# Kernel optimization log

Hardware: AMD Instinct MI355X
Metric: run time of the kernel (lower is better)

## Reference

```python
import jax, jax.numpy as jnp
import numpy as np

B, T, D, UNITS = 16, 4096, 1024, 1024


def setup_inputs() -> dict:
    key = jax.random.key(0)
    k1, k2 = jax.random.split(key)
    inputs = jax.random.normal(k1, (B, T, D), dtype=jnp.float32)
    att_keral = jax.random.normal(k2, (UNITS, D), dtype=jnp.float32) * 0.02
    return {"inputs": inputs, "att_keral": att_keral}


def reference(inputs, att_keral):
    # scores[b,t,u] = inputs[b,t,d] * att_keral[u,d] / sqrt(D)
    d = inputs.shape[-1]
    scale = 1.0 / jnp.sqrt(jnp.asarray(d, dtype=jnp.float32))
    scores = jnp.einsum('btd,ud->btu', inputs, att_keral) * scale
    # NOTE: the original computes alpha = softmax(scores) but (for isfinal=False)
    # multiplies the *scaled scores* (not alpha) back with att_keral. We reproduce
    # that exact math (alpha is dead code on this path).
    out = jnp.einsum('btu,ud->btd', scores, att_keral)
    return out
```

## Files before the change

### kernel.cpp

```cpp
#include <hip/hip_runtime.h>


typedef unsigned short u16;
typedef unsigned int u32;
typedef __bf16 bf16x8 __attribute__((ext_vector_type(8)));
typedef float f32x4 __attribute__((ext_vector_type(4)));

#define BAR() __builtin_amdgcn_s_barrier()
#define LGKM0() asm volatile("s_waitcnt lgkmcnt(0)" ::: "memory")
#define VMC(n) asm volatile("s_waitcnt vmcnt(" #n ")" ::: "memory")
#define SCHED0() __builtin_amdgcn_sched_barrier(0)

__device__ __forceinline__ u16 f2bf(float f) {
  u32 u = __float_as_uint(f);
  u += 0x7fffu + ((u >> 16) & 1u);
  return (u16)(u >> 16);
}

__device__ __forceinline__ void gload_lds16(const void* g, void* l) {
  __builtin_amdgcn_global_load_lds((const __attribute__((address_space(1))) u32*)g,
                                   (__attribute__((address_space(3))) u32*)l,
                                   16, 0, 0);
}

__device__ __forceinline__ void load2x16(const float* p, f32x4& a, f32x4& b) {
  asm volatile("global_load_dwordx4 %0, %2, off\n\t"
               "global_load_dwordx4 %1, %2, off offset:16"
               : "=&v"(a), "=&v"(b)
               : "v"(p)
               : "memory");
}

__device__ __forceinline__ bf16x8 cvt8(f32x4 a, f32x4 b) {
  bf16x8 h;
  h[0] = (__bf16)a[0]; h[1] = (__bf16)a[1]; h[2] = (__bf16)a[2]; h[3] = (__bf16)a[3];
  h[4] = (__bf16)b[0]; h[5] = (__bf16)b[1]; h[6] = (__bf16)b[2]; h[7] = (__bf16)b[3];
  return h;
}

__global__ __launch_bounds__(256) void compute_M(const float* __restrict__ W,
                                                 u16* __restrict__ Mb) {
  __shared__ float w1[32][64];
  __shared__ float w2[32][64];
  const int t = threadIdx.x;
  const int i0 = blockIdx.y * 64;
  const int j0 = blockIdx.x * 64;
  const int tx = t & 15, ty = t >> 4;
  float acc[4][4] = {};
  for (int u0 = 0; u0 < 1024; u0 += 32) {
    __syncthreads();
#pragma unroll
    for (int p = 0; p < 2; ++p) {
      int idx = p * 256 + t;
      int lu = idx >> 4, lc = (idx & 15) * 4;
      *(float4*)&w1[lu][lc] = *(const float4*)(W + (size_t)(u0 + lu) * 1024 + i0 + lc);
      *(float4*)&w2[lu][lc] = *(const float4*)(W + (size_t)(u0 + lu) * 1024 + j0 + lc);
    }
    __syncthreads();
#pragma unroll 8
    for (int u = 0; u < 32; ++u) {
      float4 a = *(const float4*)&w1[u][ty * 4];
      float4 b = *(const float4*)&w2[u][tx * 4];
      float av[4] = {a.x, a.y, a.z, a.w};
      float bv[4] = {b.x, b.y, b.z, b.w};
#pragma unroll
      for (int e = 0; e < 4; ++e)
#pragma unroll
        for (int f = 0; f < 4; ++f)
          acc[e][f] += av[e] * bv[f];
    }
  }
  const float s = 0.03125f;
#pragma unroll
  for (int e = 0; e < 4; ++e) {
    ushort4 v;
    v.x = f2bf(acc[e][0] * s);
    v.y = f2bf(acc[e][1] * s);
    v.z = f2bf(acc[e][2] * s);
    v.w = f2bf(acc[e][3] * s);
    *(ushort4*)(Mb + (size_t)(i0 + ty * 4 + e) * 1024 + j0 + tx * 4) = v;
  }
}

__global__ __launch_bounds__(512, 4) void gemm_xm(const float* __restrict__ X,
                                                  const u16* __restrict__ Mb,
                                                  float* __restrict__ out) {
  __shared__ u16 lA[2][8192];
  __shared__ u16 lB[3][4096];

  const int p = blockIdx.x;
  const int wg = (p & 7) * 256 + (p >> 3);
  const int bm = wg >> 3;
  const int bn = wg & 7;
  const size_t r0 = (size_t)bm * 256;
  const int c0 = bn * 128;

  const int t = threadIdx.x;
  const int lane = t & 63;
  const int w = t >> 6;
  const int wr = w >> 1, wc = w & 1;
  const int fr = lane & 15;
  const int kc = lane >> 4;

  const int srow = t >> 2;
  const int scl = t & 3;
  const int csw = scl ^ ((srow >> 1) & 3);
  const float* aLo = X + (r0 + srow) * 1024 + scl * 8;
  const float* aHi = X + (r0 + 128 + srow) * 1024 + scl * 8;
  u16* wLo = &lA[0][srow * 32 + csw * 8];
  u16* wHi = &lA[0][(srow + 128) * 32 + csw * 8];
  const u16* gB = Mb + (size_t)(c0 + srow) * 1024 + csw * 8;
  const int slB = w * 512;

  f32x4 acc[4][4] = {};
  f32x4 pfa, pfb, pfc, pfd;
  f32x4 q0a, q0b, q0c, q0d;

  load2x16(aLo, q0a, q0b);
  load2x16(aHi, q0c, q0d);
  load2x16(aLo + 32, pfa, pfb);
  load2x16(aHi + 32, pfc, pfd);
  gload_lds16(gB, (void*)&lB[0][slB]);
  gload_lds16(gB + 32, (void*)&lB[1][slB]);
  VMC(1);
  SCHED0();
  *(bf16x8*)(wLo) = cvt8(q0a, q0b);
  *(bf16x8*)(wHi) = cvt8(q0c, q0d);
  LGKM0();
  BAR();

  int rbB = 0, wbB = 2;
  for (int j = 0; j < 32; ++j) {
    const u16* bA = &lA[j & 1][0];
    const u16* bB = &lB[rbB][0];

    VMC(1);
    SCHED0();
    if (j <= 30) {
      const int ab = ((j + 1) & 1) * 8192;
      *(bf16x8*)(wLo + ab) = cvt8(pfa, pfb);
      *(bf16x8*)(wHi + ab) = cvt8(pfc, pfd);
    }
    bf16x8 af[4], bf[4];
#pragma unroll
    for (int m = 0; m < 4; ++m) {
      const int row = wr * 64 + m * 16 + fr;
      const int cs = kc ^ ((row >> 1) & 3);
      af[m] = *(const bf16x8*)&bA[row * 32 + cs * 8];
    }
#pragma unroll
    for (int n = 0; n < 4; ++n) {
      const int row = wc * 64 + n * 16 + fr;
      const int cs = kc ^ ((row >> 1) & 3);
      bf[n] = *(const bf16x8*)&bB[row * 32 + cs * 8];
    }
    if (j <= 29) {
      load2x16(aLo + (j + 2) * 32, pfa, pfb);
      load2x16(aHi + (j + 2) * 32, pfc, pfd);
      gload_lds16(gB + (j + 2) * 32, (void*)&lB[wbB][slB]);
    }
    BAR();
    LGKM0();
    SCHED0();
    __builtin_amdgcn_s_setprio(1);
#pragma unroll
    for (int m = 0; m < 4; ++m)
#pragma unroll
      for (int n = 0; n < 4; ++n)
        acc[m][n] = __builtin_amdgcn_mfma_f32_16x16x32_bf16(af[m], bf[n],
                                                            acc[m][n], 0, 0, 0);
    __builtin_amdgcn_s_setprio(0);
    if (j <= 29) {
      VMC(5);
    } else if (j == 30) {
      VMC(0);
    }
    SCHED0();
    BAR();
    rbB = (rbB == 2) ? 0 : rbB + 1;
    wbB = (wbB == 2) ? 0 : wbB + 1;
  }

  const int ocol = lane & 15;
  const int orow = (lane >> 4) * 4;
#pragma unroll
  for (int m = 0; m < 4; ++m) {
    const size_t rbase = (r0 + wr * 64 + m * 16 + orow) * 1024;
#pragma unroll
    for (int n = 0; n < 4; ++n) {
      float* o = out + rbase + (c0 + wc * 64 + n * 16 + ocol);
      o[0] = acc[m][n][0];
      o[1024] = acc[m][n][1];
      o[2048] = acc[m][n][2];
      o[3072] = acc[m][n][3];
    }
  }
}

extern "C" void kernel_launch(void* const* d_in, const int* in_sizes, int n_in,
                              void* d_out, int out_size, void* d_ws, size_t ws_size,
                              hipStream_t stream) {
  const float* X = (const float*)d_in[0];
  const float* W = (const float*)d_in[1];
  float* out = (float*)d_out;
  u16* Mb = (u16*)d_ws;

  compute_M<<<dim3(16, 16), 256, 0, stream>>>(W, Mb);
  gemm_xm<<<2048, 512, 0, stream>>>(X, Mb, out);
}
```

Before: 307.9 us.

## Enlarge GEMM tile to 256x256 with 8-slot LDS ping-pong pipeline

```diff
diff --git a/kernel.cpp b/kernel.cpp
--- a/kernel.cpp
+++ b/kernel.cpp
@@ -82,110 +82,132 @@
   }
 }
 
-__global__ __launch_bounds__(512, 4) void gemm_xm(const float* __restrict__ X,
-                                                  const u16* __restrict__ Mb,
-                                                  float* __restrict__ out) {
-  __shared__ u16 lA[2][8192];
-  __shared__ u16 lB[3][4096];
+__global__ __launch_bounds__(512, 2) void gemm8p(const float* __restrict__ X,
+                                                 const u16* __restrict__ Mb,
+                                                 float* __restrict__ out) {
+  __shared__ u16 lds[8 * 8192];
 
   const int p = blockIdx.x;
-  const int wg = (p & 7) * 256 + (p >> 3);
-  const int bm = wg >> 3;
-  const int bn = wg & 7;
+  const int wg = (p & 7) * 128 + (p >> 3);
+  const int bm = wg >> 2;
+  const int bn = wg & 3;
   const size_t r0 = (size_t)bm * 256;
-  const int c0 = bn * 128;
+  const int c0 = bn * 256;
 
   const int t = threadIdx.x;
   const int lane = t & 63;
   const int w = t >> 6;
-  const int wr = w >> 1, wc = w & 1;
+  const int wr = w >> 2, wc = w & 3;
   const int fr = lane & 15;
   const int kc = lane >> 4;
 
   const int srow = t >> 2;
   const int scl = t & 3;
   const int csw = scl ^ ((srow >> 1) & 3);
-  const float* aLo = X + (r0 + srow) * 1024 + scl * 8;
-  const float* aHi = X + (r0 + 128 + srow) * 1024 + scl * 8;
-  u16* wLo = &lA[0][srow * 32 + csw * 8];
-  u16* wHi = &lA[0][(srow + 128) * 32 + csw * 8];
+  const float* aL = X + (r0 + srow) * 1024 + scl * 8;
+  const float* aH = X + (r0 + 128 + srow) * 1024 + scl * 8;
   const u16* gB = Mb + (size_t)(c0 + srow) * 1024 + csw * 8;
-  const int slB = w * 512;
-
-  f32x4 acc[4][4] = {};
-  f32x4 pfa, pfb, pfc, pfd;
-  f32x4 q0a, q0b, q0c, q0d;
-
-  load2x16(aLo, q0a, q0b);
-  load2x16(aHi, q0c, q0d);
-  load2x16(aLo + 32, pfa, pfb);
-  load2x16(aHi + 32, pfc, pfd);
-  gload_lds16(gB, (void*)&lB[0][slB]);
-  gload_lds16(gB + 32, (void*)&lB[1][slB]);
-  VMC(1);
+  const u16* gB2 = Mb + (size_t)(c0 + 128 + srow) * 1024 + csw * 8;
+  u16* wLp = lds + srow * 32 + csw * 8;
+  u16* wHp = wLp + 128 * 32;
+  u16* bDst = lds + w * 512;
+
+  f32x4 acc[8][4] = {};
+  f32x4 pend[2][4];
+  f32x4 q0[4], q1[4];
+
+  load2x16(aL + 0, q0[0], q0[1]);   load2x16(aH + 0, q0[2], q0[3]);
+  load2x16(aL + 32, q1[0], q1[1]);  load2x16(aH + 32, q1[2], q1[3]);
+  gload_lds16(gB + 0, bDst + 1 * 8192);   gload_lds16(gB2 + 0, bDst + 1 * 8192 + 4096);
+  gload_lds16(gB + 32, bDst + 3 * 8192);  gload_lds16(gB2 + 32, bDst + 3 * 8192 + 4096);
+  gload_lds16(gB + 64, bDst + 5 * 8192);  gload_lds16(gB2 + 64, bDst + 5 * 8192 + 4096);
+  load2x16(aL + 64, pend[0][0], pend[0][1]); load2x16(aH + 64, pend[0][2], pend[0][3]);
+  load2x16(aL + 96, pend[1][0], pend[1][1]); load2x16(aH + 96, pend[1][2], pend[1][3]);
+  VMC(4);
   SCHED0();
-  *(bf16x8*)(wLo) = cvt8(q0a, q0b);
-  *(bf16x8*)(wHi) = cvt8(q0c, q0d);
-  LGKM0();
+  *(bf16x8*)(wLp + 0) = cvt8(q0[0], q0[1]);
+  *(bf16x8*)(wHp + 0) = cvt8(q0[2], q0[3]);
+  *(bf16x8*)(wLp + 2 * 8192) = cvt8(q1[0], q1[1]);
+  *(bf16x8*)(wHp + 2 * 8192) = cvt8(q1[2], q1[3]);
+  LGKM0(); SCHED0();
   BAR();
 
-  int rbB = 0, wbB = 2;
-  for (int j = 0; j < 32; ++j) {
-    const u16* bA = &lA[j & 1][0];
-    const u16* bB = &lB[rbB][0];
-
-    VMC(1);
-    SCHED0();
-    if (j <= 30) {
-      const int ab = ((j + 1) & 1) * 8192;
-      *(bf16x8*)(wLo + ab) = cvt8(pfa, pfb);
-      *(bf16x8*)(wHi + ab) = cvt8(pfc, pfd);
-    }
-    bf16x8 af[4], bf[4];
-#pragma unroll
-    for (int m = 0; m < 4; ++m) {
-      const int row = wr * 64 + m * 16 + fr;
-      const int cs = kc ^ ((row >> 1) & 3);
-      af[m] = *(const bf16x8*)&bA[row * 32 + cs * 8];
-    }
-#pragma unroll
-    for (int n = 0; n < 4; ++n) {
-      const int row = wc * 64 + n * 16 + fr;
-      const int cs = kc ^ ((row >> 1) & 3);
-      bf[n] = *(const bf16x8*)&bB[row * 32 + cs * 8];
-    }
-    if (j <= 29) {
-      load2x16(aLo + (j + 2) * 32, pfa, pfb);
-      load2x16(aHi + (j + 2) * 32, pfc, pfd);
-      gload_lds16(gB + (j + 2) * 32, (void*)&lB[wbB][slB]);
-    }
-    BAR();
-    LGKM0();
-    SCHED0();
-    __builtin_amdgcn_s_setprio(1);
-#pragma unroll
-    for (int m = 0; m < 4; ++m)
-#pragma unroll
-      for (int n = 0; n < 4; ++n)
-        acc[m][n] = __builtin_amdgcn_mfma_f32_16x16x32_bf16(af[m], bf[n],
-                                                            acc[m][n], 0, 0, 0);
-    __builtin_amdgcn_s_setprio(0);
-    if (j <= 29) {
-      VMC(5);
-    } else if (j == 30) {
-      VMC(0);
-    }
-    SCHED0();
-    BAR();
-    rbB = (rbB == 2) ? 0 : rbB + 1;
-    wbB = (wbB == 2) ? 0 : wbB + 1;
+  for (int b = 0; b < 8; ++b) {
+    const bool nl = (b < 7);
+    bf16x8 bf[4];
+#pragma unroll
+    for (int f = 0; f < 8; ++f) {
+      const int kh = (f >> 1) & 1;
+      const int msub = f & 1;
+      const int slotA = (f >> 2) * 4 + kh * 2;
+      if (msub == 0) {
+        const int wslot = (f == 0) ? 4 : (f == 2) ? 6 : (f == 4) ? 0 : 2;
+        if (f < 4 || nl) {
+          *(bf16x8*)(wLp + wslot * 8192) = cvt8(pend[kh][0], pend[kh][1]);
+          *(bf16x8*)(wHp + wslot * 8192) = cvt8(pend[kh][2], pend[kh][3]);
+        }
+      }
+      bf16x8 af[4];
+#pragma unroll
+      for (int i = 0; i < 4; ++i) {
+        const int row = wr * 128 + (msub * 4 + i) * 16 + fr;
+        const int cs = kc ^ ((row >> 1) & 3);
+        af[i] = *(const bf16x8*)&lds[slotA * 8192 + row * 32 + cs * 8];
+      }
+      if (msub == 0) {
+#pragma unroll
+        for (int n = 0; n < 4; ++n) {
+          const int row = wc * 64 + n * 16 + fr;
+          const int cs = kc ^ ((row >> 1) & 3);
+          bf[n] = *(const bf16x8*)&lds[(slotA + 1) * 8192 + row * 32 + cs * 8];
+        }
+      }
+      if (msub == 0 && nl) {
+        const int koff = (2 * b + 2 + (f >> 2)) * 64 + kh * 32;
+        load2x16(aL + koff, pend[kh][0], pend[kh][1]);
+        load2x16(aH + koff, pend[kh][2], pend[kh][3]);
+      }
+      if (msub == 1) {
+        const int idx = f >> 1;
+        if (idx == 0 || nl) {
+          const int kadd = (idx == 0) ? 1 : (idx == 3) ? 3 : 2;
+          const int khb = 1 - (idx & 1);
+          const int slot_s = (idx == 0) ? 7 : 2 * idx - 1;
+          const int koffb = (2 * b + kadd) * 64 + khb * 32;
+          gload_lds16(gB + koffb, bDst + slot_s * 8192);
+          gload_lds16(gB2 + koffb, bDst + slot_s * 8192 + 4096);
+        }
+      }
+      BAR();
+      LGKM0(); SCHED0();
+      __builtin_amdgcn_s_setprio(1);
+#pragma unroll
+      for (int i = 0; i < 4; ++i)
+#pragma unroll
+        for (int n = 0; n < 4; ++n)
+          acc[msub * 4 + i][n] = __builtin_amdgcn_mfma_f32_16x16x32_bf16(
+              af[i], bf[n], acc[msub * 4 + i][n], 0, 0, 0);
+      __builtin_amdgcn_s_setprio(0);
+      if (msub == 1) {
+        const int idx = f >> 1;
+        if (nl) {
+          VMC(6);
+        } else if (idx == 0) {
+          VMC(2);
+        } else if (idx == 1) {
+          VMC(0);
+        }
+        SCHED0();
+      }
+      BAR();
+    }
   }
 
   const int ocol = lane & 15;
   const int orow = (lane >> 4) * 4;
 #pragma unroll
-  for (int m = 0; m < 4; ++m) {
-    const size_t rbase = (r0 + wr * 64 + m * 16 + orow) * 1024;
+  for (int m = 0; m < 8; ++m) {
+    const size_t rbase = (r0 + wr * 128 + m * 16 + orow) * 1024;
 #pragma unroll
     for (int n = 0; n < 4; ++n) {
       float* o = out + rbase + (c0 + wc * 64 + n * 16 + ocol);
@@ -206,5 +228,5 @@
   u16* Mb = (u16*)d_ws;
 
   compute_M<<<dim3(16, 16), 256, 0, stream>>>(W, Mb);
-  gemm_xm<<<2048, 512, 0, stream>>>(X, Mb, out);
-}
+  gemm8p<<<1024, 512, 0, stream>>>(X, Mb, out);
+}
```

New measurement: 267.6 us. 1.15x faster.

## Enlarge GEMM tile to 256x256 with 4-stage LDS ring and single barrier

Applied to the files above, without the earlier changes.

```diff
diff --git a/kernel.cpp b/kernel.cpp
--- a/kernel.cpp
+++ b/kernel.cpp
@@ -82,110 +82,114 @@
   }
 }
 
-__global__ __launch_bounds__(512, 4) void gemm_xm(const float* __restrict__ X,
-                                                  const u16* __restrict__ Mb,
-                                                  float* __restrict__ out) {
-  __shared__ u16 lA[2][8192];
-  __shared__ u16 lB[3][4096];
+__global__ __launch_bounds__(512, 2) void gemm1p(const float* __restrict__ X,
+                                                 const u16* __restrict__ Mb,
+                                                 float* __restrict__ out) {
+  __shared__ u16 lA[4][8192];
+  __shared__ u16 lB[4][8192];
 
   const int p = blockIdx.x;
-  const int wg = (p & 7) * 256 + (p >> 3);
-  const int bm = wg >> 3;
-  const int bn = wg & 7;
+  const int wg = (p & 7) * 128 + (p >> 3);
+  const int bm = wg >> 2;
+  const int bn = wg & 3;
   const size_t r0 = (size_t)bm * 256;
-  const int c0 = bn * 128;
+  const int c0 = bn * 256;
 
   const int t = threadIdx.x;
   const int lane = t & 63;
   const int w = t >> 6;
-  const int wr = w >> 1, wc = w & 1;
+  const int wr = w >> 2, wc = w & 3;
   const int fr = lane & 15;
   const int kc = lane >> 4;
 
   const int srow = t >> 2;
   const int scl = t & 3;
   const int csw = scl ^ ((srow >> 1) & 3);
-  const float* aLo = X + (r0 + srow) * 1024 + scl * 8;
-  const float* aHi = X + (r0 + 128 + srow) * 1024 + scl * 8;
-  u16* wLo = &lA[0][srow * 32 + csw * 8];
-  u16* wHi = &lA[0][(srow + 128) * 32 + csw * 8];
+  const float* aL = X + (r0 + srow) * 1024 + scl * 8;
+  const float* aH = X + (r0 + 128 + srow) * 1024 + scl * 8;
   const u16* gB = Mb + (size_t)(c0 + srow) * 1024 + csw * 8;
-  const int slB = w * 512;
-
-  f32x4 acc[4][4] = {};
+  const u16* gB2 = Mb + (size_t)(c0 + 128 + srow) * 1024 + csw * 8;
+  u16* wLp = &lA[0][srow * 32 + csw * 8];
+  u16* wHp = wLp + 128 * 32;
+  u16* bDst = &lB[0][w * 512];
+
+  f32x4 acc[8][4] = {};
   f32x4 pfa, pfb, pfc, pfd;
-  f32x4 q0a, q0b, q0c, q0d;
-
-  load2x16(aLo, q0a, q0b);
-  load2x16(aHi, q0c, q0d);
-  load2x16(aLo + 32, pfa, pfb);
-  load2x16(aHi + 32, pfc, pfd);
-  gload_lds16(gB, (void*)&lB[0][slB]);
-  gload_lds16(gB + 32, (void*)&lB[1][slB]);
-  VMC(1);
+  f32x4 q0a, q0b, q0c, q0d, q1a, q1b, q1c, q1d;
+
+  load2x16(aL + 0, q0a, q0b);   load2x16(aH + 0, q0c, q0d);
+  load2x16(aL + 32, q1a, q1b);  load2x16(aH + 32, q1c, q1d);
+  gload_lds16(gB + 0, bDst);
+  gload_lds16(gB2 + 0, bDst + 4096);
+  load2x16(aL + 64, pfa, pfb);  load2x16(aH + 64, pfc, pfd);
+  gload_lds16(gB + 32, bDst + 8192);
+  gload_lds16(gB2 + 32, bDst + 8192 + 4096);
+  VMC(6);
   SCHED0();
-  *(bf16x8*)(wLo) = cvt8(q0a, q0b);
-  *(bf16x8*)(wHi) = cvt8(q0c, q0d);
-  LGKM0();
+  *(bf16x8*)(wLp + 0 * 8192) = cvt8(q0a, q0b);
+  *(bf16x8*)(wHp + 0 * 8192) = cvt8(q0c, q0d);
+  *(bf16x8*)(wLp + 1 * 8192) = cvt8(q1a, q1b);
+  *(bf16x8*)(wHp + 1 * 8192) = cvt8(q1c, q1d);
+  LGKM0(); SCHED0();
   BAR();
 
-  int rbB = 0, wbB = 2;
   for (int j = 0; j < 32; ++j) {
-    const u16* bA = &lA[j & 1][0];
-    const u16* bB = &lB[rbB][0];
-
-    VMC(1);
+    const u16* bA = &lA[j & 3][0];
+    const u16* bB = &lB[j & 3][0];
+    const int sb = (j + 2) & 3;
+
+    VMC(2);
     SCHED0();
-    if (j <= 30) {
-      const int ab = ((j + 1) & 1) * 8192;
-      *(bf16x8*)(wLo + ab) = cvt8(pfa, pfb);
-      *(bf16x8*)(wHi + ab) = cvt8(pfc, pfd);
-    }
-    bf16x8 af[4], bf[4];
-#pragma unroll
-    for (int m = 0; m < 4; ++m) {
-      const int row = wr * 64 + m * 16 + fr;
-      const int cs = kc ^ ((row >> 1) & 3);
-      af[m] = *(const bf16x8*)&bA[row * 32 + cs * 8];
-    }
+    if (j <= 29) {
+      *(bf16x8*)(wLp + sb * 8192) = cvt8(pfa, pfb);
+      *(bf16x8*)(wHp + sb * 8192) = cvt8(pfc, pfd);
+    }
+    bf16x8 bf[4], af[8];
 #pragma unroll
     for (int n = 0; n < 4; ++n) {
       const int row = wc * 64 + n * 16 + fr;
       const int cs = kc ^ ((row >> 1) & 3);
       bf[n] = *(const bf16x8*)&bB[row * 32 + cs * 8];
     }
+#pragma unroll
+    for (int m = 0; m < 8; ++m) {
+      const int row = wr * 128 + m * 16 + fr;
+      const int cs = kc ^ ((row >> 1) & 3);
+      af[m] = *(const bf16x8*)&bA[row * 32 + cs * 8];
+    }
+    if (j <= 28) {
+      load2x16(aL + (j + 3) * 32, pfa, pfb);
+      load2x16(aH + (j + 3) * 32, pfc, pfd);
+    }
     if (j <= 29) {
-      load2x16(aLo + (j + 2) * 32, pfa, pfb);
-      load2x16(aHi + (j + 2) * 32, pfc, pfd);
-      gload_lds16(gB + (j + 2) * 32, (void*)&lB[wbB][slB]);
-    }
-    BAR();
-    LGKM0();
-    SCHED0();
+      gload_lds16(gB + (j + 2) * 32, (void*)(bDst + sb * 8192));
+      gload_lds16(gB2 + (j + 2) * 32, (void*)(bDst + sb * 8192 + 4096));
+    }
     __builtin_amdgcn_s_setprio(1);
 #pragma unroll
-    for (int m = 0; m < 4; ++m)
+    for (int m = 0; m < 8; ++m)
 #pragma unroll
       for (int n = 0; n < 4; ++n)
         acc[m][n] = __builtin_amdgcn_mfma_f32_16x16x32_bf16(af[m], bf[n],
                                                             acc[m][n], 0, 0, 0);
     __builtin_amdgcn_s_setprio(0);
-    if (j <= 29) {
-      VMC(5);
+    if (j <= 28) {
+      VMC(6);
+    } else if (j == 29) {
+      VMC(2);
     } else if (j == 30) {
       VMC(0);
     }
+    LGKM0();
     SCHED0();
     BAR();
-    rbB = (rbB == 2) ? 0 : rbB + 1;
-    wbB = (wbB == 2) ? 0 : wbB + 1;
   }
 
   const int ocol = lane & 15;
   const int orow = (lane >> 4) * 4;
 #pragma unroll
-  for (int m = 0; m < 4; ++m) {
-    const size_t rbase = (r0 + wr * 64 + m * 16 + orow) * 1024;
+  for (int m = 0; m < 8; ++m) {
+    const size_t rbase = (r0 + wr * 128 + m * 16 + orow) * 1024;
 #pragma unroll
     for (int n = 0; n < 4; ++n) {
       float* o = out + rbase + (c0 + wc * 64 + n * 16 + ocol);
@@ -206,5 +210,5 @@
   u16* Mb = (u16*)d_ws;
 
   compute_M<<<dim3(16, 16), 256, 0, stream>>>(W, Mb);
-  gemm_xm<<<2048, 512, 0, stream>>>(X, Mb, out);
-}
+  gemm1p<<<1024, 512, 0, stream>>>(X, Mb, out);
+}
```

Result: faster. 268.1 us (-12.9%).
